# Kernel optimization log

Measured on AMD Instinct MI355X. Metric: run time of the kernel, lower is better.

Reference implementation:

```python
import jax, jax.numpy as jnp
import numpy as np

EMB = 128   # embedding_dim
ND = 128    # node_dim
B = 64      # graphs in batch
NN = 500    # n_nodes per graph
N = B * NN  # total nodes = 32000
E = 256000  # edges per edge set
M = 20      # history length in input_


def _lin_params(key, out_dim, in_dim, bias=True):
    k1, k2 = jax.random.split(key)
    s = 1.0 / np.sqrt(in_dim)
    w = jax.random.uniform(k1, (out_dim, in_dim), jnp.float32, -s, s)
    if bias:
        b = jax.random.uniform(k2, (out_dim,), jnp.float32, -s, s)
        return w, b
    return w


def setup_inputs() -> dict:
    key = jax.random.key(0)
    ks = jax.random.split(key, 40)
    inp = {}
    inp["state_"] = jax.random.normal(ks[0], (B, ND), jnp.float32)
    inp["input_"] = jax.random.normal(ks[1], (B, M, EMB), jnp.float32)
    inp["x"] = jax.random.normal(ks[2], (N, EMB), jnp.float32)
    inp["e_n"] = jax.random.randint(ks[3], (2, E), 0, N)
    inp["e_r0"] = jax.random.randint(ks[4], (2, E), 0, N)
    inp["e_r1"] = jax.random.randint(ks[5], (2, E), 0, N)
    inp["n_nodes"] = NN
    # GRU-like params
    inp["win"] = _lin_params(ks[6], ND, EMB, bias=False)
    inp["wz"], inp["bz"] = _lin_params(ks[7], ND, 2 * ND)
    inp["wr"], inp["br"] = _lin_params(ks[8], ND, 2 * ND)
    inp["wh"], inp["bh"] = _lin_params(ks[9], ND, 2 * ND)
    # GAT params: lin (out,in)+bias, attn (out, 2*out)+bias
    inp["g0_lw"], inp["g0_lb"] = _lin_params(ks[10], ND, EMB)
    inp["g0_aw"], inp["g0_ab"] = _lin_params(ks[11], ND, 2 * ND)
    inp["g1_lw"], inp["g1_lb"] = _lin_params(ks[12], ND, ND)
    inp["g1_aw"], inp["g1_ab"] = _lin_params(ks[13], ND, 2 * ND)
    inp["g2_lw"], inp["g2_lb"] = _lin_params(ks[14], ND, ND)
    inp["g2_aw"], inp["g2_ab"] = _lin_params(ks[15], ND, 2 * ND)
    inp["gn_lw"], inp["gn_lb"] = _lin_params(ks[16], ND, ND)
    inp["gn_aw"], inp["gn_ab"] = _lin_params(ks[17], ND, 2 * ND)
    # heads
    inp["pw"], inp["pb"] = _lin_params(ks[18], 1, ND)
    inp["mw"], inp["mb"] = _lin_params(ks[19], 1, ND)
    inp["sw"], inp["sb"] = _lin_params(ks[20], 1, ND)
    return inp


def gat_conv(x, ei, lw, lb, aw, ab, slope=0.2):
    """PyG GATConv variant: lin -> per-edge attn(cat(x_i,x_j)) -> leaky_relu ->
    per-dst segment softmax (per channel) -> scatter-add of x_j*alpha."""
    n = x.shape[0]
    sl = jnp.arange(n)
    src = jnp.concatenate([ei[0], sl])   # j (source)
    dst = jnp.concatenate([ei[1], sl])   # i (target; softmax + aggregation index)
    h = x @ lw.T + lb                    # [N, ND]
    hi = h[dst]                          # x_i  [E', ND]
    hj = h[src]                          # x_j  [E', ND]
    a = jnp.concatenate([hi, hj], axis=-1) @ aw.T + ab
    a = jax.nn.leaky_relu(a, slope)
    amax = jax.ops.segment_max(a, dst, num_segments=n)
    e = jnp.exp(a - amax[dst])
    denom = jax.ops.segment_sum(e, dst, num_segments=n)
    alpha = e / (denom[dst] + 1e-16)
    return jax.ops.segment_sum(hj * alpha, dst, num_segments=n)


def reference(state_, input_, x, e_n, e_r0, e_r1, n_nodes,
              win, wz, bz, wr, br, wh, bh,
              g0_lw, g0_lb, g0_aw, g0_ab,
              g1_lw, g1_lb, g1_aw, g1_ab,
              g2_lw, g2_lb, g2_aw, g2_ab,
              gn_lw, gn_lb, gn_aw, gn_ab,
              pw, pb, mw, mb, sw, sb):
    # GRU-like gated state update
    st = state_.reshape(-1, ND)
    inp = input_.reshape(st.shape[0], -1, EMB)
    i = jnp.mean(inp @ win.T, axis=1)              # [B, ND]
    si = jnp.concatenate([st, i], axis=-1)
    z = jax.nn.sigmoid(si @ wz.T + bz)
    r = jax.nn.sigmoid(si @ wr.T + br)
    hc = jnp.tanh(jnp.concatenate([r * st, i], axis=-1) @ wh.T + bh)
    h = (1 - z) * st + z * hc                      # [B, ND]

    # Stacked GAT layers
    g0 = gat_conv(x, e_n, g0_lw, g0_lb, g0_aw, g0_ab)
    g1 = gat_conv(g0, e_r1, g1_lw, g1_lb, g1_aw, g1_ab)
    g2 = gat_conv(g1, e_r1, g1_lw, g1_lb, g1_aw, g1_ab)
    g3 = gat_conv(g2, e_n, gn_lw, gn_lb, gn_aw, gn_ab) + g0
    g4 = gat_conv(g3, e_r0, g2_lw, g2_lb, g2_aw, g2_ab)
    g5 = gat_conv(g4, e_r0, g2_lw, g2_lb, g2_aw, g2_ab)
    gx = gat_conv(g5, e_n, gn_lw, gn_lb, gn_aw, gn_ab) + g3

    xg = gx.reshape(-1, n_nodes, ND)               # [B, NN, ND]
    xt = xg[:, 1:]                                 # skip depot node
    scores = (xt @ pw.T + pb)[..., 0]              # [B, NN-1]
    probs = jax.nn.softmax(scores, axis=-1)        # Categorical params
    a = jax.nn.elu((xt @ mw.T + mb)[..., 0]) + 2   # Beta alpha
    b = jax.nn.elu(jnp.abs((xt @ sw.T + sb)[..., 0])) + 2  # Beta beta
    return (h, probs, a, b)
```

## Files before the change

### kernel.cpp

```cpp
#include <hip/hip_runtime.h>
#include <hip/hip_bf16.h>

#define ND 128
#define EMB 128
#define BATCH 64
#define MM 20
#define NN 500
#define RPAD 8

typedef short bf16x8 __attribute__((ext_vector_type(8)));
typedef float f32x4 __attribute__((ext_vector_type(4)));

__device__ __forceinline__ float bf2f(unsigned short u) {
    union { unsigned int i; float f; } x; x.i = ((unsigned int)u) << 16; return x.f;
}
__device__ __forceinline__ unsigned short f2bf(float f) {
    union { float f; unsigned int i; } x; x.f = f;
    unsigned int r = x.i + 0x7fffu + ((x.i >> 16) & 1u);
    return (unsigned short)(r >> 16);
}
__device__ __forceinline__ float2 bfpair(unsigned int p) {
    union { unsigned int i; float f; } a, b;
    a.i = p << 16; b.i = p & 0xffff0000u;
    return make_float2(a.f, b.f);
}

struct EdgePtrs { const int* e[3]; };

__global__ void edge_hist3(EdgePtrs ep, int* __restrict__ cnt, int E, int N) {
    int li = blockIdx.y;
    const int* dst = ep.e[li] + E;
    int e = blockIdx.x * blockDim.x + threadIdx.x;
    if (e < E) atomicAdd(&cnt[(size_t)li * N + dst[e]], 1);
}

__global__ void exscan3(const int* __restrict__ cnt, int* __restrict__ rowptr, int n) {
    __shared__ int wsum[16];
    __shared__ int woff[16];
    int li = blockIdx.x;
    const int4* c4 = (const int4*)(cnt + (size_t)li * n);
    int* rp = rowptr + (size_t)li * (n + RPAD);
    int t = threadIdx.x;
    int lane = t & 63, wid = t >> 6;
    int n4 = n >> 2;

    int4 v[8];
    int s = 0;
#pragma unroll
    for (int i = 0; i < 8; ++i) {
        int idx = t * 8 + i;
        if (idx < n4) v[i] = c4[idx];
        else { v[i].x = v[i].y = v[i].z = v[i].w = 0; }
    }
#pragma unroll
    for (int i = 0; i < 8; ++i) s += v[i].x + v[i].y + v[i].z + v[i].w;

    int ps = s;
#pragma unroll
    for (int d = 1; d < 64; d <<= 1) {
        int u = __shfl_up(ps, d, 64);
        if (lane >= d) ps += u;
    }
    if (lane == 63) wsum[wid] = ps;
    __syncthreads();
    if (t == 0) {
        int r = 0;
        for (int i = 0; i < 16; ++i) { woff[i] = r; r += wsum[i]; }
    }
    __syncthreads();
    int run = woff[wid] + ps - s;
    int4* rp4 = (int4*)rp;
#pragma unroll
    for (int i = 0; i < 8; ++i) {
        int idx = t * 8 + i;
        if (idx < n4) {
            int4 o;
            o.x = run; run += v[i].x;
            o.y = run; run += v[i].y;
            o.z = run; run += v[i].z;
            o.w = run; run += v[i].w;
            rp4[idx] = o;
        }
    }
    if (t == (n - 1) / 32) rp[n] = run;
}

__global__ void edge_scatter3(EdgePtrs ep, const int* __restrict__ rowptr, int* __restrict__ cnt,
                              int* __restrict__ col, int E, int N) {
    int li = blockIdx.y;
    const int* src = ep.e[li];
    const int* dst = src + E;
    const int* rp = rowptr + (size_t)li * (N + RPAD);
    int e = blockIdx.x * blockDim.x + threadIdx.x;
    if (e < E) {
        int d = dst[e];
        int p = atomicSub(&cnt[(size_t)li * N + d], 1) - 1;
        __builtin_nontemporal_store(src[e], &col[(size_t)li * E + rp[d] + p]);
    }
}

struct WcPtrs {
    const float* lw[4]; const float* lb[4]; const float* aw[4]; const float* ab[4];
    unsigned short* Whi[4]; unsigned short* Wlo[4]; float* Bf[4];
};

__global__ void make_wc4(WcPtrs p) {
    int set = blockIdx.y;
    const float* lw = p.lw[set]; const float* lb = p.lb[set];
    const float* aw = p.aw[set]; const float* ab = p.ab[set];
    int n = blockIdx.x;
    int e = threadIdx.x;
    float w;
    if (n < 128) {
        w = lw[n * 128 + e];
    } else if (n < 256) {
        int ni = n - 128; float s = 0.f;
        for (int k = 0; k < 128; ++k) s += aw[ni * 256 + k] * lw[k * 128 + e];
        w = s;
    } else {
        int nj = n - 256; float s = 0.f;
        for (int k = 0; k < 128; ++k) s += aw[nj * 256 + 128 + k] * lw[k * 128 + e];
        w = s;
    }
    unsigned short hi = f2bf(w);
    p.Whi[set][n * 128 + e] = hi;
    p.Wlo[set][n * 128 + e] = f2bf(w - bf2f(hi));
    if (e == 0) {
        float b;
        if (n < 128) b = lb[n];
        else if (n < 256) {
            int ni = n - 128; float s = ab[ni];
            for (int k = 0; k < 128; ++k) s += aw[ni * 256 + k] * lb[k];
            b = s;
        } else {
            int nj = n - 256; float s = 0.f;
            for (int k = 0; k < 128; ++k) s += aw[nj * 256 + 128 + k] * lb[k];
            b = s;
        }
        p.Bf[set][n] = b;
    }
}

__launch_bounds__(384)
__global__ void lin_fused(const float* __restrict__ X,
                          const unsigned short* __restrict__ Whi,
                          const unsigned short* __restrict__ Wlo,
                          const float* __restrict__ bias,
                          void* __restrict__ hu, int M) {
    const int slab = threadIdx.x >> 6;
    const int lane = threadIdx.x & 63;
    const int r16 = lane & 15;
    const int quad = lane >> 4;

    unsigned short* hu16 = (unsigned short*)hu;
    float* huf = (float*)hu;

    const unsigned short* Wh = Whi + (size_t)slab * 64 * 128;
    const unsigned short* Wl = Wlo + (size_t)slab * 64 * 128;
    bf16x8 wh[4][4], wl[4][4];
#pragma unroll
    for (int nt = 0; nt < 4; ++nt)
#pragma unroll
        for (int ks = 0; ks < 4; ++ks) {
            wh[nt][ks] = *(const bf16x8*)(Wh + (nt * 16 + r16) * 128 + ks * 32 + quad * 8);
            wl[nt][ks] = *(const bf16x8*)(Wl + (nt * 16 + r16) * 128 + ks * 32 + quad * 8);
        }
    float bv[4];
#pragma unroll
    for (int nt = 0; nt < 4; ++nt) bv[nt] = bias[slab * 64 + nt * 16 + r16];

    const int mt_count = M >> 4;
    for (int mt = blockIdx.x; mt < mt_count; mt += gridDim.x) {
        bf16x8 ah[4], al[4];
#pragma unroll
        for (int ks = 0; ks < 4; ++ks) {
            const float* xp = X + (size_t)(mt * 16 + r16) * 128 + ks * 32 + quad * 8;
            float4 v0 = *(const float4*)xp;
            float4 v1 = *(const float4*)(xp + 4);
            float v[8] = {v0.x, v0.y, v0.z, v0.w, v1.x, v1.y, v1.z, v1.w};
#pragma unroll
            for (int j = 0; j < 8; ++j) {
                unsigned short h = f2bf(v[j]);
                ah[ks][j] = (short)h;
                al[ks][j] = (short)f2bf(v[j] - bf2f(h));
            }
        }
#pragma unroll
        for (int nt = 0; nt < 4; ++nt) {
            f32x4 acc = {bv[nt], bv[nt], bv[nt], bv[nt]};
#pragma unroll
            for (int ks = 0; ks < 4; ++ks) {
                acc = __builtin_amdgcn_mfma_f32_16x16x32_bf16(ah[ks], wh[nt][ks], acc, 0, 0, 0);
                acc = __builtin_amdgcn_mfma_f32_16x16x32_bf16(al[ks], wh[nt][ks], acc, 0, 0, 0);
                acc = __builtin_amdgcn_mfma_f32_16x16x32_bf16(ah[ks], wl[nt][ks], acc, 0, 0, 0);
            }
            int col = slab * 64 + nt * 16 + r16;
#pragma unroll
            for (int r = 0; r < 4; ++r) {
                size_t row = (size_t)(mt * 16 + quad * 4 + r);
                if (slab < 2) {
                    int c = col;
                    hu16[row * 512 + ((c & ~1) << 1) + (c & 1)] = f2bf(acc[r]);
                } else if (slab < 4) {
                    int c = col - 128;
                    huf[row * 256 + 128 + c] = acc[r];
                } else {
                    int c = col - 256;
                    hu16[row * 512 + ((c & ~1) << 1) + 2 + (c & 1)] = f2bf(acc[r]);
                }
            }
        }
    }
}

__global__ void gat_agg(const void* __restrict__ hu,
                        const int* __restrict__ rowptr, const int* __restrict__ col,
                        const float* __restrict__ resid,
                        float* __restrict__ out, int N) {
    int wid = (int)((blockIdx.x * blockDim.x + threadIdx.x) >> 6);
    if (wid >= N) return;
    int lane = threadIdx.x & 63;
    const uint2* P = (const uint2*)hu;
    const float2* U = (const float2*)hu;

    float2 uiv = U[(size_t)wid * 128 + 64 + lane];
    uint2 sp = P[(size_t)wid * 128 + lane];
    float2 hs = bfpair(sp.x);
    float2 ujs = bfpair(sp.y);

    float a0 = uiv.x + ujs.x; a0 = a0 > 0.f ? a0 : 0.2f * a0;
    float a1 = uiv.y + ujs.y; a1 = a1 > 0.f ? a1 : 0.2f * a1;
    float m0 = a0, m1 = a1, l0 = 1.f, l1 = 1.f;
    float acc0 = hs.x, acc1 = hs.y;

#define AGG_STEP(pk)                                                      \
    {                                                                     \
        float2 hj = bfpair(pk.x);                                         \
        float2 uj = bfpair(pk.y);                                         \
        float b0 = uiv.x + uj.x; b0 = b0 > 0.f ? b0 : 0.2f * b0;          \
        float b1 = uiv.y + uj.y; b1 = b1 > 0.f ? b1 : 0.2f * b1;          \
        float n0 = fmaxf(m0, b0), n1 = fmaxf(m1, b1);                     \
        float s0 = __expf(m0 - n0), s1 = __expf(m1 - n1);                 \
        float p0 = __expf(b0 - n0), p1 = __expf(b1 - n1);                 \
        l0 = l0 * s0 + p0;            l1 = l1 * s1 + p1;                  \
        acc0 = acc0 * s0 + hj.x * p0; acc1 = acc1 * s1 + hj.y * p1;       \
        m0 = n0; m1 = n1;                                                 \
    }

    int e = rowptr[wid], end = rowptr[wid + 1];
    for (; e + 4 <= end; e += 4) {
        int sA = col[e], sB = col[e + 1], sC = col[e + 2], sD = col[e + 3];
        uint2 pA = P[(size_t)sA * 128 + lane];
        uint2 pB = P[(size_t)sB * 128 + lane];
        uint2 pC = P[(size_t)sC * 128 + lane];
        uint2 pD = P[(size_t)sD * 128 + lane];
        AGG_STEP(pA);
        AGG_STEP(pB);
        AGG_STEP(pC);
        AGG_STEP(pD);
    }
    for (; e < end; ++e) {
        int sA = col[e];
        uint2 pA = P[(size_t)sA * 128 + lane];
        AGG_STEP(pA);
    }
#undef AGG_STEP

    float o0 = acc0 / (l0 + 1e-16f);
    float o1 = acc1 / (l1 + 1e-16f);
    if (resid) {
        float2 rv = ((const float2*)resid)[(size_t)wid * 64 + lane];
        o0 += rv.x; o1 += rv.y;
    }
    ((float2*)out)[(size_t)wid * 64 + lane] = make_float2(o0, o1);
}

__global__ void gru_kernel(const float* __restrict__ st_, const float* __restrict__ in_,
                           const float* __restrict__ win,
                           const float* __restrict__ wz, const float* __restrict__ bz,
                           const float* __restrict__ wr, const float* __restrict__ br,
                           const float* __restrict__ wh, const float* __restrict__ bh,
                           float* __restrict__ out) {
    __shared__ float sst[ND], sib[EMB], si[ND], srs[ND];
    int b = blockIdx.x, d = threadIdx.x;
    float s = 0.f;
    for (int m = 0; m < MM; ++m) s += in_[((size_t)b * MM + m) * EMB + d];
    sib[d] = s * (1.0f / MM);
    sst[d] = st_[b * ND + d];
    __syncthreads();
    float iv = 0.f;
    for (int e = 0; e < EMB; ++e) iv += sib[e] * win[d * EMB + e];
    si[d] = iv;
    __syncthreads();
    float za = bz[d], ra = br[d];
    for (int e = 0; e < ND; ++e) {
        za += sst[e] * wz[d * 2 * ND + e] + si[e] * wz[d * 2 * ND + ND + e];
        ra += sst[e] * wr[d * 2 * ND + e] + si[e] * wr[d * 2 * ND + ND + e];
    }
    float z = 1.f / (1.f + __expf(-za));
    float r = 1.f / (1.f + __expf(-ra));
    srs[d] = r * sst[d];
    __syncthreads();
    float ha = bh[d];
    for (int e = 0; e < ND; ++e)
        ha += srs[e] * wh[d * 2 * ND + e] + si[e] * wh[d * 2 * ND + ND + e];
    float hc = tanhf(ha);
    out[b * ND + d] = (1.f - z) * sst[d] + z * hc;
}

__global__ void heads_dots(const float* __restrict__ gx,
                           const float* __restrict__ pw_,
                           const float* __restrict__ mw_, const float* __restrict__ mb_,
                           const float* __restrict__ sw_, const float* __restrict__ sbias_,
                           float* __restrict__ scores, float* __restrict__ out) {
    int t = blockIdx.x;
    int lane = threadIdx.x & 63;
    int b = blockIdx.y * 4 + (threadIdx.x >> 6);
    const float2* g2 = (const float2*)gx;
    float2 pwv = ((const float2*)pw_)[lane];
    float2 mwv = ((const float2*)mw_)[lane];
    float2 swv = ((const float2*)sw_)[lane];
    int node = b * NN + 1 + t;
    float2 xv = g2[(size_t)node * 64 + lane];
    float dp = xv.x * pwv.x + xv.y * pwv.y;
    float dm = xv.x * mwv.x + xv.y * mwv.y;
    float ds = xv.x * swv.x + xv.y * swv.y;
    for (int off = 32; off; off >>= 1) {
        dp += __shfl_xor(dp, off);
        dm += __shfl_xor(dm, off);
        ds += __shfl_xor(ds, off);
    }
    if (lane == 0) {
        scores[(size_t)b * (NN - 1) + t] = dp;
        float av = dm + mb_[0]; av = av > 0.f ? av : (__expf(av) - 1.f);
        float bv = fabsf(ds + sbias_[0]);
        float* oA = out + BATCH * ND + (size_t)BATCH * (NN - 1);
        float* oB = oA + (size_t)BATCH * (NN - 1);
        oA[(size_t)b * (NN - 1) + t] = av + 2.f;
        oB[(size_t)b * (NN - 1) + t] = bv + 2.f;
    }
}

__global__ void heads_softmax(const float* __restrict__ scores, float* __restrict__ out) {
    __shared__ float scs[NN - 1], red[256];
    int b = blockIdx.x, tid = threadIdx.x;
    float mx = -1e30f;
    for (int t = tid; t < NN - 1; t += 256) { float v = scores[(size_t)b * (NN - 1) + t]; scs[t] = v; mx = fmaxf(mx, v); }
    red[tid] = mx; __syncthreads();
    for (int off = 128; off; off >>= 1) { if (tid < off) red[tid] = fmaxf(red[tid], red[tid + off]); __syncthreads(); }
    mx = red[0]; __syncthreads();
    float sum = 0.f;
    for (int t = tid; t < NN - 1; t += 256) { float e = __expf(scs[t] - mx); scs[t] = e; sum += e; }
    red[tid] = sum; __syncthreads();
    for (int off = 128; off; off >>= 1) { if (tid < off) red[tid] += red[tid + off]; __syncthreads(); }
    float inv = 1.0f / red[0];
    float* oP = out + BATCH * ND + (size_t)b * (NN - 1);
    for (int t = tid; t < NN - 1; t += 256) oP[t] = scs[t] * inv;
}

extern "C" void kernel_launch(void* const* d_in, const int* in_sizes, int n_in,
                              void* d_out, int out_size, void* d_ws, size_t ws_size,
                              hipStream_t stream) {
    const float* state_ = (const float*)d_in[0];
    const float* input_ = (const float*)d_in[1];
    const float* x      = (const float*)d_in[2];
    const int* e_n  = (const int*)d_in[3];
    const int* e_r0 = (const int*)d_in[4];
    const int* e_r1 = (const int*)d_in[5];
    const float* win = (const float*)d_in[7];
    const float* wz  = (const float*)d_in[8];
    const float* bz  = (const float*)d_in[9];
    const float* wr  = (const float*)d_in[10];
    const float* br  = (const float*)d_in[11];
    const float* wh  = (const float*)d_in[12];
    const float* bh  = (const float*)d_in[13];
    const float* pw = (const float*)d_in[30];
    const float* mw = (const float*)d_in[32];
    const float* mb = (const float*)d_in[33];
    const float* sw = (const float*)d_in[34];
    const float* sb = (const float*)d_in[35];
    float* out = (float*)d_out;

    const int E = in_sizes[3] / 2;
    const int N = in_sizes[2] / EMB;

    char* w = (char*)d_ws;
    auto alloc = [&](size_t bytes) { char* p = w; w += (bytes + 255) & ~(size_t)255; return p; };
    int* rpbase = (int*)alloc(3 * (size_t)(N + RPAD) * sizeof(int));
    int* colbase = (int*)alloc(3 * (size_t)E * sizeof(int));
    int* tmp = (int*)alloc(3 * (size_t)N * sizeof(int));
    unsigned short* Whi[4]; unsigned short* Wlo[4]; float* Bf[4];
    for (int i = 0; i < 4; ++i) {
        Whi[i] = (unsigned short*)alloc(384 * 128 * 2);
        Wlo[i] = (unsigned short*)alloc(384 * 128 * 2);
        Bf[i]  = (float*)alloc(384 * 4);
    }
    void* hu = (void*)alloc((size_t)N * 1024);
    float* ga = (float*)alloc((size_t)N * 128 * 4);
    float* gb = (float*)alloc((size_t)N * 128 * 4);
    float* gc = (float*)alloc((size_t)N * 128 * 4);
    float* scores = (float*)alloc((size_t)BATCH * (NN - 1) * 4);

    EdgePtrs ep; ep.e[0] = e_n; ep.e[1] = e_r0; ep.e[2] = e_r1;

    hipMemsetAsync(tmp, 0, 3 * (size_t)N * sizeof(int), stream);
    edge_hist3<<<dim3((E + 255) / 256, 3), 256, 0, stream>>>(ep, tmp, E, N);
    exscan3<<<3, 1024, 0, stream>>>(tmp, rpbase, N);
    edge_scatter3<<<dim3((E + 255) / 256, 3), 256, 0, stream>>>(ep, rpbase, tmp, colbase, E, N);

    WcPtrs wp;
    wp.lw[0] = (const float*)d_in[14]; wp.lb[0] = (const float*)d_in[15];
    wp.aw[0] = (const float*)d_in[16]; wp.ab[0] = (const float*)d_in[17];
    wp.lw[1] = (const float*)d_in[18]; wp.lb[1] = (const float*)d_in[19];
    wp.aw[1] = (const float*)d_in[20]; wp.ab[1] = (const float*)d_in[21];
    wp.lw[2] = (const float*)d_in[22]; wp.lb[2] = (const float*)d_in[23];
    wp.aw[2] = (const float*)d_in[24]; wp.ab[2] = (const float*)d_in[25];
    wp.lw[3] = (const float*)d_in[26]; wp.lb[3] = (const float*)d_in[27];
    wp.aw[3] = (const float*)d_in[28]; wp.ab[3] = (const float*)d_in[29];
    for (int i = 0; i < 4; ++i) { wp.Whi[i] = Whi[i]; wp.Wlo[i] = Wlo[i]; wp.Bf[i] = Bf[i]; }
    make_wc4<<<dim3(384, 4), 128, 0, stream>>>(wp);

    gru_kernel<<<BATCH, ND, 0, stream>>>(state_, input_, win, wz, bz, wr, br, wh, bh, out);

    auto conv = [&](const float* in, int csr_i, int wi, const float* resid, float* o) {
        lin_fused<<<256, 384, 0, stream>>>(in, Whi[wi], Wlo[wi], Bf[wi], hu, N);
        gat_agg<<<(N * 64) / 256, 256, 0, stream>>>(hu, rpbase + (size_t)csr_i * (N + RPAD),
                                                    colbase + (size_t)csr_i * E, resid, o, N);
    };

    conv(x,  0, 0, nullptr, ga);
    conv(ga, 2, 1, nullptr, gb);
    conv(gb, 2, 1, nullptr, gc);
    conv(gc, 0, 3, ga,      gb);
    conv(gb, 1, 2, nullptr, gc);
    conv(gc, 1, 2, nullptr, ga);
    conv(ga, 0, 3, gb,      gc);

    heads_dots<<<dim3(NN - 1, 16), 256, 0, stream>>>(gc, pw, mw, mb, sw, sb, scores, out);
    heads_softmax<<<BATCH, 256, 0, stream>>>(scores, out);
}
```

Before: 661.0 us.

## Process two nodes per wavefront in GAT aggregation with 16-byte lane loads

The aggregation kernel now assigns each half-wave (32 lanes) to one destination node, with every lane handling four channels through uint4/float4 loads instead of two channels through uint2 loads. The edge loop runs over two edges per iteration under a wave-wide predicate, so the two halves stay in step even when their degrees differ. This halves the number of waves and widens memory transactions, at the cost of idle lanes when neighbouring nodes have uneven degree. It also doubles the lin_fused grid and replaces the nontemporal store in the CSR scatter with a plain store.

```diff
diff --git a/kernel.cpp b/kernel.cpp
--- a/kernel.cpp
+++ b/kernel.cpp
@@ -95,7 +95,7 @@
     if (e < E) {
         int d = dst[e];
         int p = atomicSub(&cnt[(size_t)li * N + d], 1) - 1;
-        __builtin_nontemporal_store(src[e], &col[(size_t)li * E + rp[d] + p]);
+        col[(size_t)li * E + rp[d] + p] = src[e];
     }
 }
 
@@ -217,62 +217,77 @@
                         const int* __restrict__ rowptr, const int* __restrict__ col,
                         const float* __restrict__ resid,
                         float* __restrict__ out, int N) {
-    int wid = (int)((blockIdx.x * blockDim.x + threadIdx.x) >> 6);
-    if (wid >= N) return;
+    int wave = (int)((blockIdx.x * blockDim.x + threadIdx.x) >> 6);
     int lane = threadIdx.x & 63;
-    const uint2* P = (const uint2*)hu;
-    const float2* U = (const float2*)hu;
-
-    float2 uiv = U[(size_t)wid * 128 + 64 + lane];
-    uint2 sp = P[(size_t)wid * 128 + lane];
-    float2 hs = bfpair(sp.x);
-    float2 ujs = bfpair(sp.y);
-
-    float a0 = uiv.x + ujs.x; a0 = a0 > 0.f ? a0 : 0.2f * a0;
-    float a1 = uiv.y + ujs.y; a1 = a1 > 0.f ? a1 : 0.2f * a1;
-    float m0 = a0, m1 = a1, l0 = 1.f, l1 = 1.f;
-    float acc0 = hs.x, acc1 = hs.y;
-
-#define AGG_STEP(pk)                                                      \
-    {                                                                     \
-        float2 hj = bfpair(pk.x);                                         \
-        float2 uj = bfpair(pk.y);                                         \
-        float b0 = uiv.x + uj.x; b0 = b0 > 0.f ? b0 : 0.2f * b0;          \
-        float b1 = uiv.y + uj.y; b1 = b1 > 0.f ? b1 : 0.2f * b1;          \
+    int half = lane >> 5;
+    int sub = lane & 31;
+    int node = wave * 2 + half;
+    if (node >= N) return;
+
+    const uint4* P4 = (const uint4*)hu;
+    const float4* U4 = (const float4*)hu;
+
+    float4 ui = U4[(size_t)node * 64 + 32 + sub];
+    uint4 sp = P4[(size_t)node * 64 + sub];
+
+    float m0, m1, m2, m3, l0 = 1.f, l1 = 1.f, l2 = 1.f, l3 = 1.f;
+    float acc0, acc1, acc2, acc3;
+    {
+        float2 hA = bfpair(sp.x), uA = bfpair(sp.y);
+        float2 hB = bfpair(sp.z), uB = bfpair(sp.w);
+        float b0 = ui.x + uA.x; b0 = b0 > 0.f ? b0 : 0.2f * b0;
+        float b1 = ui.y + uA.y; b1 = b1 > 0.f ? b1 : 0.2f * b1;
+        float b2 = ui.z + uB.x; b2 = b2 > 0.f ? b2 : 0.2f * b2;
+        float b3 = ui.w + uB.y; b3 = b3 > 0.f ? b3 : 0.2f * b3;
+        m0 = b0; m1 = b1; m2 = b2; m3 = b3;
+        acc0 = hA.x; acc1 = hA.y; acc2 = hB.x; acc3 = hB.y;
+    }
+
+#define AGG_STEP(pk, valid)                                               \
+    if (valid) {                                                          \
+        float2 hA = bfpair(pk.x), uA = bfpair(pk.y);                      \
+        float2 hB = bfpair(pk.z), uB = bfpair(pk.w);                      \
+        float b0 = ui.x + uA.x; b0 = b0 > 0.f ? b0 : 0.2f * b0;           \
+        float b1 = ui.y + uA.y; b1 = b1 > 0.f ? b1 : 0.2f * b1;           \
+        float b2 = ui.z + uB.x; b2 = b2 > 0.f ? b2 : 0.2f * b2;           \
+        float b3 = ui.w + uB.y; b3 = b3 > 0.f ? b3 : 0.2f * b3;           \
         float n0 = fmaxf(m0, b0), n1 = fmaxf(m1, b1);                     \
+        float n2 = fmaxf(m2, b2), n3 = fmaxf(m3, b3);                     \
         float s0 = __expf(m0 - n0), s1 = __expf(m1 - n1);                 \
+        float s2 = __expf(m2 - n2), s3 = __expf(m3 - n3);                 \
         float p0 = __expf(b0 - n0), p1 = __expf(b1 - n1);                 \
-        l0 = l0 * s0 + p0;            l1 = l1 * s1 + p1;                  \
-        acc0 = acc0 * s0 + hj.x * p0; acc1 = acc1 * s1 + hj.y * p1;       \
-        m0 = n0; m1 = n1;                                                 \
-    }
-
-    int e = rowptr[wid], end = rowptr[wid + 1];
-    for (; e + 4 <= end; e += 4) {
-        int sA = col[e], sB = col[e + 1], sC = col[e + 2], sD = col[e + 3];
-        uint2 pA = P[(size_t)sA * 128 + lane];
-        uint2 pB = P[(size_t)sB * 128 + lane];
-        uint2 pC = P[(size_t)sC * 128 + lane];
-        uint2 pD = P[(size_t)sD * 128 + lane];
-        AGG_STEP(pA);
-        AGG_STEP(pB);
-        AGG_STEP(pC);
-        AGG_STEP(pD);
-    }
-    for (; e < end; ++e) {
-        int sA = col[e];
-        uint2 pA = P[(size_t)sA * 128 + lane];
-        AGG_STEP(pA);
+        float p2 = __expf(b2 - n2), p3 = __expf(b3 - n3);                 \
+        l0 = l0 * s0 + p0; l1 = l1 * s1 + p1;                             \
+        l2 = l2 * s2 + p2; l3 = l3 * s3 + p3;                             \
+        acc0 = acc0 * s0 + hA.x * p0; acc1 = acc1 * s1 + hA.y * p1;       \
+        acc2 = acc2 * s2 + hB.x * p2; acc3 = acc3 * s3 + hB.y * p3;       \
+        m0 = n0; m1 = n1; m2 = n2; m3 = n3;                               \
+    }
+
+    int e = rowptr[node], end = rowptr[node + 1];
+    while (__any(e < end)) {
+        int ec = end - 1; if (ec < 0) ec = 0;
+        int e0 = e < ec ? e : ec;
+        int e1 = (e + 1) < ec ? (e + 1) : ec;
+        int s0i = col[e0], s1i = col[e1];
+        uint4 p0 = P4[(size_t)s0i * 64 + sub];
+        uint4 p1 = P4[(size_t)s1i * 64 + sub];
+        AGG_STEP(p0, e < end);
+        AGG_STEP(p1, e + 1 < end);
+        e += 2;
     }
 #undef AGG_STEP
 
-    float o0 = acc0 / (l0 + 1e-16f);
-    float o1 = acc1 / (l1 + 1e-16f);
+    float4 o;
+    o.x = acc0 / (l0 + 1e-16f);
+    o.y = acc1 / (l1 + 1e-16f);
+    o.z = acc2 / (l2 + 1e-16f);
+    o.w = acc3 / (l3 + 1e-16f);
     if (resid) {
-        float2 rv = ((const float2*)resid)[(size_t)wid * 64 + lane];
-        o0 += rv.x; o1 += rv.y;
-    }
-    ((float2*)out)[(size_t)wid * 64 + lane] = make_float2(o0, o1);
+        float4 rv = ((const float4*)resid)[(size_t)node * 32 + sub];
+        o.x += rv.x; o.y += rv.y; o.z += rv.z; o.w += rv.w;
+    }
+    ((float4*)out)[(size_t)node * 32 + sub] = o;
 }
 
 __global__ void gru_kernel(const float* __restrict__ st_, const float* __restrict__ in_,
@@ -423,9 +438,11 @@
     gru_kernel<<<BATCH, ND, 0, stream>>>(state_, input_, win, wz, bz, wr, br, wh, bh, out);
 
     auto conv = [&](const float* in, int csr_i, int wi, const float* resid, float* o) {
-        lin_fused<<<256, 384, 0, stream>>>(in, Whi[wi], Wlo[wi], Bf[wi], hu, N);
-        gat_agg<<<(N * 64) / 256, 256, 0, stream>>>(hu, rpbase + (size_t)csr_i * (N + RPAD),
-                                                    colbase + (size_t)csr_i * E, resid, o, N);
+        lin_fused<<<512, 384, 0, stream>>>(in, Whi[wi], Wlo[wi], Bf[wi], hu, N);
+        int waves = (N + 1) / 2;
+        gat_agg<<<(waves * 64 + 255) / 256, 256, 0, stream>>>(
+            hu, rpbase + (size_t)csr_i * (N + RPAD),
+            colbase + (size_t)csr_i * E, resid, o, N);
     };
 
     conv(x,  0, 0, nullptr, ga);
```

New measurement: 740.2 us. 12.0% more time.
